# Kernel tuning notes

Measured on AMD Instinct MI355X. Metric: run time of the kernel, lower is better.

## Reference

```python
import jax, jax.numpy as jnp
import numpy as np

N_NODES = 100000
N_EDGES = 1600000
D = 64
N_LAYERS = 3
N_GRAPHS = 128
BN_EPS = 1e-5


def setup_inputs() -> dict:
    key = jax.random.key(0)
    k_x, k_e, k_b, k_w = jax.random.split(key, 4)
    x = jax.random.normal(k_x, (N_NODES, D), dtype=jnp.float32)
    edge_index = jax.random.randint(k_e, (2, N_EDGES), 0, N_NODES, dtype=jnp.int64)
    batch = jnp.sort(jax.random.randint(k_b, (N_NODES,), 0, N_GRAPHS, dtype=jnp.int64))
    Ws = jax.random.normal(k_w, (N_LAYERS, D, D), dtype=jnp.float32) * (1.0 / np.sqrt(D))
    bs = jnp.zeros((N_LAYERS, D), dtype=jnp.float32)
    gammas = jnp.ones((N_LAYERS, D), dtype=jnp.float32)
    betas = jnp.zeros((N_LAYERS, D), dtype=jnp.float32)
    return {"x": x, "edge_index": edge_index, "batch": batch,
            "Ws": Ws, "bs": bs, "gammas": gammas, "betas": betas}


def reference(x, edge_index, batch, Ws, bs, gammas, betas):
    N = x.shape[0]
    # GCN: add self-loops, symmetric normalization deg^{-1/2}_src * deg^{-1/2}_dst
    loop = jnp.arange(N, dtype=edge_index.dtype)
    src = jnp.concatenate([edge_index[0], loop])  # [E+N]
    dst = jnp.concatenate([edge_index[1], loop])
    deg = jax.ops.segment_sum(jnp.ones_like(dst, dtype=x.dtype), dst, num_segments=N)
    dinv = jnp.where(deg > 0, jax.lax.rsqrt(deg), 0.0)
    norm = dinv[src] * dinv[dst]  # [E+N]

    h = x
    for l in range(N_LAYERS):
        t = h @ Ws[l]                                    # [N,D] dense transform
        msg = t[src] * norm[:, None]                     # gather + scale [E+N,D]
        t = jax.ops.segment_sum(msg, dst, num_segments=N) + bs[l]
        # BatchNorm1d (training-style batch statistics, biased variance)
        mean = jnp.mean(t, axis=0)
        var = jnp.mean((t - mean) ** 2, axis=0)
        t = (t - mean) * jax.lax.rsqrt(var + BN_EPS) * gammas[l] + betas[l]
        h = jax.nn.relu(t)

    # global mean pool over graphs
    sums = jax.ops.segment_sum(h, batch, num_segments=N_GRAPHS)        # [G,D]
    counts = jax.ops.segment_sum(jnp.ones((N,), dtype=h.dtype), batch, num_segments=N_GRAPHS)
    return sums / jnp.maximum(counts, 1.0)[:, None]
```

## Files before the change

kernel.cpp:

```cpp
#include <hip/hip_runtime.h>
#include <hip/hip_bf16.h>

typedef __hip_bfloat16 bf16;
typedef short bf16x8 __attribute__((ext_vector_type(8)));
typedef float f32x4 __attribute__((ext_vector_type(4)));

#define NN 100000
#define NE 1600000
#define DD 64
#define NL 3
#define NG 128
#define BN_EPS 1e-5f
#define SCAN_BLK 98
#define TILE_ROWS 64
#define LSW 72
#define NT ((NN + TILE_ROWS - 1) / TILE_ROWS)
#define GB_NODES 48
#define GB_BLOCKS ((NN + GB_NODES - 1) / GB_NODES)
#define ECAP 1664
#define CSW_CAP (NE + 7 * NN)

__global__ __launch_bounds__(256) void detect_kernel(const int* __restrict__ ei,
                                                     const int* __restrict__ batch,
                                                     int* __restrict__ flags) {
    __shared__ int s_e, s_b;
    if (threadIdx.x == 0) { s_e = 0; s_b = 0; }
    __syncthreads();
    for (int i = threadIdx.x; i < 512; i += 256) {
        if (ei[2 * i + 1] != 0) atomicOr(&s_e, 1);
        if (batch[NN - 1024 + 2 * i + 1] != 0) atomicOr(&s_b, 1);
    }
    __syncthreads();
    if (threadIdx.x == 0) { flags[0] = s_e; flags[1] = s_b; }
}

__device__ __forceinline__ int ld_src(const int* ei, int e, int is32) {
    return is32 ? ei[e] : ei[2 * e];
}
__device__ __forceinline__ int ld_dst(const int* ei, int e, int is32) {
    return is32 ? ei[NE + e] : ei[2 * NE + 2 * e];
}
__device__ __forceinline__ int ld_batch(const int* b, int n, int is32) {
    return is32 ? b[n] : b[2 * n];
}
__device__ __forceinline__ float bf2f(unsigned short u) {
    return __uint_as_float(((unsigned int)u) << 16);
}
__device__ __forceinline__ unsigned short f2bf(float x) {
    bf16 b = __float2bfloat16(x);
    return *reinterpret_cast<unsigned short*>(&b);
}
__device__ __forceinline__ void split_bf16(float x, unsigned short& hi, unsigned short& lo) {
    hi = f2bf(x);
    lo = f2bf(x - bf2f(hi));
}
__device__ __forceinline__ int pad8(int d) { return (d + 7) & ~7; }

__global__ __launch_bounds__(256) void deg_kernel(const int* __restrict__ ei,
                                                  const int* __restrict__ flags,
                                                  int* __restrict__ deg_cnt) {
    int is32 = flags[0];
    int e = blockIdx.x * 256 + threadIdx.x;
    if (e < NE) atomicAdd(&deg_cnt[ld_dst(ei, e, is32)], 1);
}

__global__ __launch_bounds__(256) void scan_part_kernel(const int* __restrict__ deg_cnt,
                                                        int* __restrict__ blocksum,
                                                        float* __restrict__ dinv) {
    __shared__ int s[256];
    int base = blockIdx.x * 1024 + threadIdx.x * 4;
    int t = 0;
    if (base < NN) {
        int4 v = *(const int4*)(deg_cnt + base);
        t = pad8(v.x) + pad8(v.y) + pad8(v.z) + pad8(v.w);
        float4 dv = make_float4(rsqrtf((float)v.x + 1.f), rsqrtf((float)v.y + 1.f),
                                rsqrtf((float)v.z + 1.f), rsqrtf((float)v.w + 1.f));
        *(float4*)(dinv + base) = dv;
    }
    s[threadIdx.x] = t;
    __syncthreads();
    for (int off = 128; off > 0; off >>= 1) {
        if (threadIdx.x < off) s[threadIdx.x] += s[threadIdx.x + off];
        __syncthreads();
    }
    if (threadIdx.x == 0) blocksum[blockIdx.x] = s[0];
}

__global__ __launch_bounds__(256) void scan_write_kernel(int* __restrict__ deg_cnt,
                                                         const int* __restrict__ blocksum,
                                                         int* __restrict__ rowptr) {
    __shared__ int sb[128];
    __shared__ int s[256];
    if (threadIdx.x < 128)
        sb[threadIdx.x] = (threadIdx.x < SCAN_BLK) ? blocksum[threadIdx.x] : 0;
    __syncthreads();
    for (int off = 1; off < 128; off <<= 1) {
        int a = 0;
        if (threadIdx.x < 128 && threadIdx.x >= off) a = sb[threadIdx.x - off];
        __syncthreads();
        if (threadIdx.x < 128) sb[threadIdx.x] += a;
        __syncthreads();
    }
    int blockpre = (blockIdx.x == 0) ? 0 : sb[blockIdx.x - 1];
    if (blockIdx.x == SCAN_BLK - 1 && threadIdx.x == 0)
        rowptr[NN] = sb[SCAN_BLK - 1];

    int base = blockIdx.x * 1024 + threadIdx.x * 4;
    int4 v = make_int4(0, 0, 0, 0);
    if (base < NN) v = *(const int4*)(deg_cnt + base);
    int p0 = pad8(v.x), p1 = pad8(v.y), p2 = pad8(v.z), p3 = pad8(v.w);
    int t = p0 + p1 + p2 + p3;
    s[threadIdx.x] = t;
    for (int off = 1; off < 256; off <<= 1) {
        __syncthreads();
        int a = (threadIdx.x >= off) ? s[threadIdx.x - off] : 0;
        __syncthreads();
        s[threadIdx.x] += a;
    }
    __syncthreads();
    int pre = blockpre + s[threadIdx.x] - t;
    if (base < NN) {
        rowptr[base] = pre;
        rowptr[base + 1] = pre + p0;
        rowptr[base + 2] = pre + p0 + p1;
        rowptr[base + 3] = pre + p0 + p1 + p2;
        *(int4*)(deg_cnt + base) = make_int4(0, 0, 0, 0);
    }
}

__global__ __launch_bounds__(256) void fill_kernel(const int* __restrict__ ei,
                                                   const int* __restrict__ flags,
                                                   const float* __restrict__ dinv,
                                                   const int* __restrict__ rowptr,
                                                   int* __restrict__ cursor,
                                                   int2* __restrict__ csw) {
    int is32 = flags[0];
    int e = blockIdx.x * 256 + threadIdx.x;
    if (e >= NE) return;
    int s = ld_src(ei, e, is32), d = ld_dst(ei, e, is32);
    int pos = rowptr[d] + atomicAdd(&cursor[d], 1);
    float w = dinv[s] * dinv[d];
    csw[pos] = make_int2(s << 7, __float_as_int(w));
}

__global__ __launch_bounds__(256) void gemm_kernel(const float* __restrict__ h,
                                                   const float* __restrict__ W,
                                                   const float* __restrict__ accum_prev,
                                                   const float* __restrict__ gamma,
                                                   const float* __restrict__ beta,
                                                   int use_bn, float alpha,
                                                   bf16* __restrict__ t,
                                                   float* __restrict__ accum_l) {
    if (blockIdx.x == 0 && threadIdx.x < 128) accum_l[threadIdx.x] = 0.f;

    __shared__ unsigned short ls_hi[TILE_ROWS * LSW];
    __shared__ unsigned short ls_lo[TILE_ROWS * LSW];
    __shared__ float ssc[DD], ssh[DD];
    int tid = threadIdx.x;
    if (tid < 64) {
        if (use_bn) {
            float S = accum_prev[tid], Q = accum_prev[64 + tid];
            float mean = S / (float)NN;
            float var = fmaxf(Q / (float)NN - mean * mean, 0.f);
            float sc = gamma[tid] * rsqrtf(var + BN_EPS);
            ssc[tid] = sc;
            ssh[tid] = beta[tid] - mean * sc;
        } else {
            ssc[tid] = 1.f;
            ssh[tid] = 0.f;
        }
    }

    int lane = tid & 63;
    int wv = tid >> 6;
    int lr = lane & 15;
    int lg = lane >> 4;

    bf16x8 bhi[2][4], blo[2][4];
#pragma unroll
    for (int ks = 0; ks < 2; ++ks)
#pragma unroll
        for (int nt = 0; nt < 4; ++nt)
#pragma unroll
            for (int e = 0; e < 8; ++e) {
                float wval = W[(ks * 32 + lg * 8 + e) * DD + nt * 16 + lr];
                unsigned short hi, lo;
                split_bf16(wval, hi, lo);
                bhi[ks][nt][e] = (short)hi;
                blo[ks][nt][e] = (short)lo;
            }
    __syncthreads();

    for (int tile = blockIdx.x; tile < NT; tile += gridDim.x) {
        int row0 = tile * TILE_ROWS;
        int nrows = min(TILE_ROWS, NN - row0);
#pragma unroll
        for (int it = 0; it < 4; ++it) {
            int flat = (tid + it * 256) * 4;
            int gflat = row0 * DD + flat;
            if (gflat < NN * DD) {
                float4 hv = *(const float4*)(h + gflat);
                int c0 = flat & 63;
                float4 s4 = *(const float4*)(ssc + c0);
                float4 b4 = *(const float4*)(ssh + c0);
                float x0 = hv.x * s4.x + b4.x;
                float x1 = hv.y * s4.y + b4.y;
                float x2 = hv.z * s4.z + b4.z;
                float x3 = hv.w * s4.w + b4.w;
                x0 = fmaxf(x0, x0 * alpha);
                x1 = fmaxf(x1, x1 * alpha);
                x2 = fmaxf(x2, x2 * alpha);
                x3 = fmaxf(x3, x3 * alpha);
                unsigned short h0, l0, h1, l1, h2, l2, h3, l3;
                split_bf16(x0, h0, l0);
                split_bf16(x1, h1, l1);
                split_bf16(x2, h2, l2);
                split_bf16(x3, h3, l3);
                int row = flat >> 6;
                *(ushort4*)(ls_hi + row * LSW + c0) = make_ushort4(h0, h1, h2, h3);
                *(ushort4*)(ls_lo + row * LSW + c0) = make_ushort4(l0, l1, l2, l3);
            }
        }
        __syncthreads();

        f32x4 acc[4];
#pragma unroll
        for (int nt = 0; nt < 4; ++nt) acc[nt] = (f32x4){0.f, 0.f, 0.f, 0.f};

#pragma unroll
        for (int ks = 0; ks < 2; ++ks) {
            int aoff = (wv * 16 + lr) * LSW + ks * 32 + lg * 8;
            bf16x8 a_hi = *(const bf16x8*)(ls_hi + aoff);
            bf16x8 a_lo = *(const bf16x8*)(ls_lo + aoff);
#pragma unroll
            for (int nt = 0; nt < 4; ++nt) {
                acc[nt] = __builtin_amdgcn_mfma_f32_16x16x32_bf16(a_hi, bhi[ks][nt],
                                                                  acc[nt], 0, 0, 0);
                acc[nt] = __builtin_amdgcn_mfma_f32_16x16x32_bf16(a_hi, blo[ks][nt],
                                                                  acc[nt], 0, 0, 0);
                acc[nt] = __builtin_amdgcn_mfma_f32_16x16x32_bf16(a_lo, bhi[ks][nt],
                                                                  acc[nt], 0, 0, 0);
            }
        }
        __syncthreads();

#pragma unroll
        for (int nt = 0; nt < 4; ++nt)
#pragma unroll
            for (int rg = 0; rg < 4; ++rg) {
                int orow = wv * 16 + lg * 4 + rg;
                ls_hi[orow * LSW + nt * 16 + lr] = f2bf(acc[nt][rg]);
            }
        __syncthreads();
#pragma unroll
        for (int it = 0; it < 2; ++it) {
            int flat8 = (tid + it * 256) * 8;
            int row = flat8 >> 6, c = flat8 & 63;
            if (row < nrows) {
                uint4 v = *(const uint4*)(ls_hi + row * LSW + c);
                *(uint4*)((unsigned short*)t + (size_t)(row0 + row) * DD + c) = v;
            }
        }
        __syncthreads();
    }
}

__device__ __forceinline__ void batch8(const int2* __restrict__ ep, int j,
                                       const char* __restrict__ tbase, int f2,
                                       float& acc) {
    int2 a[8];
    unsigned short r[8];
#pragma unroll
    for (int u = 0; u < 8; ++u) a[u] = ep[j + u];
#pragma unroll
    for (int u = 0; u < 8; ++u)
        r[u] = *(const unsigned short*)(tbase + (unsigned)(a[u].x + f2));
#pragma unroll
    for (int u = 0; u < 8; ++u) acc += bf2f(r[u]) * __int_as_float(a[u].y);
}

__device__ __forceinline__ void batch8x2(const int2* __restrict__ ep, int jA, int jB,
                                         const char* __restrict__ tbase, int f2,
                                         float& accA, float& accB) {
    int2 aA[8], aB[8];
    unsigned short rA[8], rB[8];
#pragma unroll
    for (int u = 0; u < 8; ++u) { aA[u] = ep[jA + u]; aB[u] = ep[jB + u]; }
#pragma unroll
    for (int u = 0; u < 8; ++u) {
        rA[u] = *(const unsigned short*)(tbase + (unsigned)(aA[u].x + f2));
        rB[u] = *(const unsigned short*)(tbase + (unsigned)(aB[u].x + f2));
    }
#pragma unroll
    for (int u = 0; u < 8; ++u) {
        accA += bf2f(rA[u]) * __int_as_float(aA[u].y);
        accB += bf2f(rB[u]) * __int_as_float(aB[u].y);
    }
}

__device__ __forceinline__ void batch8x4(const int2* __restrict__ ep, int jA, int jB,
                                         int jC, int jD,
                                         const char* __restrict__ tbase, int f2,
                                         float& accA, float& accB, float& accC,
                                         float& accD) {
    int2 aA[8], aB[8], aC[8], aD[8];
    unsigned short rA[8], rB[8], rC[8], rD[8];
#pragma unroll
    for (int u = 0; u < 8; ++u) {
        aA[u] = ep[jA + u];
        aB[u] = ep[jB + u];
        aC[u] = ep[jC + u];
        aD[u] = ep[jD + u];
    }
#pragma unroll
    for (int u = 0; u < 8; ++u) {
        rA[u] = *(const unsigned short*)(tbase + (unsigned)(aA[u].x + f2));
        rB[u] = *(const unsigned short*)(tbase + (unsigned)(aB[u].x + f2));
        rC[u] = *(const unsigned short*)(tbase + (unsigned)(aC[u].x + f2));
        rD[u] = *(const unsigned short*)(tbase + (unsigned)(aD[u].x + f2));
    }
#pragma unroll
    for (int u = 0; u < 8; ++u) {
        accA += bf2f(rA[u]) * __int_as_float(aA[u].y);
        accB += bf2f(rB[u]) * __int_as_float(aB[u].y);
        accC += bf2f(rC[u]) * __int_as_float(aC[u].y);
        accD += bf2f(rD[u]) * __int_as_float(aD[u].y);
    }
}

__device__ __forceinline__ void run_quad(const int2* __restrict__ ep,
                                         const char* __restrict__ tbase, int f2,
                                         int jA, int eA, int jB, int eB,
                                         int jC, int eC, int jD, int eD,
                                         float& accA, float& accB, float& accC,
                                         float& accD) {
    while (jA < eA && jB < eB && jC < eC && jD < eD) {
        batch8x4(ep, jA, jB, jC, jD, tbase, f2, accA, accB, accC, accD);
        jA += 8; jB += 8; jC += 8; jD += 8;
    }
    while (jA < eA && jB < eB) { batch8x2(ep, jA, jB, tbase, f2, accA, accB); jA += 8; jB += 8; }
    while (jC < eC && jD < eD) { batch8x2(ep, jC, jD, tbase, f2, accC, accD); jC += 8; jD += 8; }
    while (jA < eA && jC < eC) { batch8x2(ep, jA, jC, tbase, f2, accA, accC); jA += 8; jC += 8; }
    while (jA < eA && jD < eD) { batch8x2(ep, jA, jD, tbase, f2, accA, accD); jA += 8; jD += 8; }
    while (jB < eB && jC < eC) { batch8x2(ep, jB, jC, tbase, f2, accB, accC); jB += 8; jC += 8; }
    while (jB < eB && jD < eD) { batch8x2(ep, jB, jD, tbase, f2, accB, accD); jB += 8; jD += 8; }
    while (jA < eA) { batch8(ep, jA, tbase, f2, accA); jA += 8; }
    while (jB < eB) { batch8(ep, jB, tbase, f2, accB); jB += 8; }
    while (jC < eC) { batch8(ep, jC, tbase, f2, accC); jC += 8; }
    while (jD < eD) { batch8(ep, jD, tbase, f2, accD); jD += 8; }
}

__global__ __launch_bounds__(256) void gather_kernel(const bf16* __restrict__ t,
                                                     const float* __restrict__ dinv,
                                                     const float* __restrict__ bias,
                                                     const int* __restrict__ rowptr,
                                                     const int2* __restrict__ csw,
                                                     float* __restrict__ h,
                                                     float* __restrict__ accum_l) {
    __shared__ int2 se[ECAP];
    __shared__ int srp[GB_NODES + 1];
    __shared__ float s_sum[256], s_sq[256];

    int f = threadIdx.x & 63;
    int wv = threadIdx.x >> 6;
    int nb0 = blockIdx.x * GB_NODES;
    int nloc = min(GB_NODES, NN - nb0);

    for (int i = threadIdx.x; i <= nloc; i += 256) srp[i] = rowptr[nb0 + i];
    __syncthreads();
    int ebase = srp[0];
    int nE = srp[nloc] - ebase;
    bool staged = (nE <= ECAP);
    int ncap = min(nE, ECAP);
    for (int i = threadIdx.x; i < ncap; i += 256) se[i] = csw[ebase + i];
    __syncthreads();

    const char* tbase = (const char*)t;
    int f2 = f * 2;
    const unsigned short* tf = (const unsigned short*)t + f;
    float bb = bias[f];
    float sum = 0.f, sq = 0.f;

    for (int q = wv; 4 * q < nloc; q += 4) {
        int d0 = 4 * q;
        int nA = nb0 + d0, nB = nA + 1, nC = nA + 2, nD = nA + 3;
        float diA = dinv[nA], diB = dinv[nB], diC = dinv[nC], diD = dinv[nD];
        float accA = bf2f(tf[(size_t)nA * DD]) * diA * diA + bb;
        float accB = bf2f(tf[(size_t)nB * DD]) * diB * diB + bb;
        float accC = bf2f(tf[(size_t)nC * DD]) * diC * diC + bb;
        float accD = bf2f(tf[(size_t)nD * DD]) * diD * diD + bb;
        int jA = srp[d0] - ebase, eA = srp[d0 + 1] - ebase;
        int jB = eA, eB = srp[d0 + 2] - ebase;
        int jC = eB, eC = srp[d0 + 3] - ebase;
        int jD = eC, eD = srp[d0 + 4] - ebase;

        if (staged)
            run_quad(se, tbase, f2, jA, eA, jB, eB, jC, eC, jD, eD, accA, accB, accC, accD);
        else
            run_quad(csw + ebase, tbase, f2, jA, eA, jB, eB, jC, eC, jD, eD,
                     accA, accB, accC, accD);

        h[(size_t)nA * DD + f] = accA;
        h[(size_t)nB * DD + f] = accB;
        h[(size_t)nC * DD + f] = accC;
        h[(size_t)nD * DD + f] = accD;
        sum += accA + accB + accC + accD;
        sq += accA * accA + accB * accB + accC * accC + accD * accD;
    }
    s_sum[threadIdx.x] = sum;
    s_sq[threadIdx.x] = sq;
    __syncthreads();
    if (threadIdx.x < 64) {
        sum = s_sum[f] + s_sum[64 + f] + s_sum[128 + f] + s_sum[192 + f];
        sq = s_sq[f] + s_sq[64 + f] + s_sq[128 + f] + s_sq[192 + f];
        atomicAdd(&accum_l[f], sum);
        atomicAdd(&accum_l[64 + f], sq);
    }
}

#define POOL_CHUNK 128
__global__ __launch_bounds__(256) void pool_kernel(const float* __restrict__ hraw,
                                                   const float* __restrict__ accum_l,
                                                   const float* __restrict__ gamma,
                                                   const float* __restrict__ beta,
                                                   const int* __restrict__ batch,
                                                   const int* __restrict__ flags,
                                                   float* __restrict__ pool,
                                                   float* __restrict__ counts) {
    __shared__ float ssc[64], ssh[64];
    if (threadIdx.x < 64) {
        float S = accum_l[threadIdx.x], Q = accum_l[64 + threadIdx.x];
        float mean = S / (float)NN;
        float var = fmaxf(Q / (float)NN - mean * mean, 0.f);
        float sc = gamma[threadIdx.x] * rsqrtf(var + BN_EPS);
        ssc[threadIdx.x] = sc;
        ssh[threadIdx.x] = beta[threadIdx.x] - mean * sc;
    }
    __syncthreads();
    int is32 = flags[1];
    int f = threadIdx.x & 63, rg = threadIdx.x >> 6;
    float sc = ssc[f], sh = ssh[f];
    int base = blockIdx.x * POOL_CHUNK;
    float acc = 0.f, cnt = 0.f;
    int cur = -1;
    for (int i = rg; i < POOL_CHUNK; i += 4) {
        int n = base + i;
        if (n >= NN) break;
        int g = ld_batch(batch, n, is32);
        if (g != cur) {
            if (cur >= 0) {
                atomicAdd(&pool[cur * DD + f], acc);
                if (f == 0) atomicAdd(&counts[cur], cnt);
            }
            acc = 0.f;
            cnt = 0.f;
            cur = g;
        }
        acc += fmaxf(hraw[(size_t)n * DD + f] * sc + sh, 0.f);
        cnt += 1.f;
    }
    if (cur >= 0) {
        atomicAdd(&pool[cur * DD + f], acc);
        if (f == 0) atomicAdd(&counts[cur], cnt);
    }
}

__global__ __launch_bounds__(256) void final_kernel(const float* __restrict__ pool,
                                                    const float* __restrict__ counts,
                                                    float* __restrict__ out) {
    int i = blockIdx.x * 256 + threadIdx.x;
    if (i < NG * DD) {
        int g = i >> 6;
        out[i] = pool[i] / fmaxf(counts[g], 1.0f);
    }
}

extern "C" void kernel_launch(void* const* d_in, const int* in_sizes, int n_in,
                              void* d_out, int out_size, void* d_ws, size_t ws_size,
                              hipStream_t stream) {
    const float* x = (const float*)d_in[0];
    const int* edge_index = (const int*)d_in[1];
    const int* batch = (const int*)d_in[2];
    const float* Ws = (const float*)d_in[3];
    const float* bs = (const float*)d_in[4];
    const float* gammas = (const float*)d_in[5];
    const float* betas = (const float*)d_in[6];
    float* out = (float*)d_out;

    float* h = (float*)d_ws;
    bf16* t = (bf16*)(h + (size_t)NN * DD);
    int2* csw = (int2*)(t + (size_t)NN * DD);
    float* dinv = (float*)(csw + CSW_CAP);
    int* deg_cnt = (int*)(dinv + NN);
    float* pool = (float*)(deg_cnt + NN);
    float* counts = pool + NG * DD;
    int* rowptr = (int*)(counts + NG);
    float* accum = (float*)(rowptr + NN + 1);
    int* flags = (int*)(accum + NL * 128);
    int* blocksum = flags + 2;

    hipMemsetAsync(deg_cnt, 0, (NN + NG * DD + NG) * sizeof(float), stream);
    hipMemsetAsync(csw, 0, (size_t)CSW_CAP * sizeof(int2), stream);

    detect_kernel<<<1, 256, 0, stream>>>(edge_index, batch, flags);
    deg_kernel<<<(NE + 255) / 256, 256, 0, stream>>>(edge_index, flags, deg_cnt);
    scan_part_kernel<<<SCAN_BLK, 256, 0, stream>>>(deg_cnt, blocksum, dinv);
    scan_write_kernel<<<SCAN_BLK, 256, 0, stream>>>(deg_cnt, blocksum, rowptr);
    fill_kernel<<<(NE + 255) / 256, 256, 0, stream>>>(edge_index, flags, dinv, rowptr,
                                                      deg_cnt, csw);

    for (int l = 0; l < NL; ++l) {
        const float* hin = (l == 0) ? x : h;
        float alpha = (l == 0) ? 1.0f : 0.0f;
        gemm_kernel<<<NT, 256, 0, stream>>>(hin, Ws + (size_t)l * DD * DD,
                                            accum + (l - 1 >= 0 ? l - 1 : 0) * 128,
                                            gammas + (l - 1 >= 0 ? l - 1 : 0) * DD,
                                            betas + (l - 1 >= 0 ? l - 1 : 0) * DD,
                                            (l > 0) ? 1 : 0, alpha, t, accum + l * 128);
        gather_kernel<<<GB_BLOCKS, 256, 0, stream>>>(t, dinv, bs + l * DD, rowptr, csw, h,
                                                     accum + l * 128);
    }

    pool_kernel<<<(NN + POOL_CHUNK - 1) / POOL_CHUNK, 256, 0, stream>>>(
        h, accum + 2 * 128, gammas + 2 * DD, betas + 2 * DD, batch, flags, pool, counts);
    final_kernel<<<(NG * DD + 255) / 256, 256, 0, stream>>>(pool, counts, out);
}
```

Baseline: 557.8 us.

## Factor GCN normalization into GEMM prescale and gather postscale, drop edge weights

Splits the symmetric normalization dinv[s]*dinv[d]: the GEMM epilogue scales each output row by dinv of the source, and the gather multiplies the summed neighbour row by dinv of the destination. This removes the per-edge weight, halving the CSR edge array to one int per edge and letting the gather load indices as int4 and do plain adds instead of FMAs with weights. Padding entries now point to a zeroed row placed before t, via the index offset s+1 and a tbase shifted back by 128 bytes. The cost is one extra per-row multiply in the GEMM and slightly different rounding, since the prescaled value is stored in bf16.

```diff
diff --git a/kernel.cpp b/kernel.cpp
--- a/kernel.cpp
+++ b/kernel.cpp
@@ -130,21 +130,20 @@
 
 __global__ __launch_bounds__(256) void fill_kernel(const int* __restrict__ ei,
                                                    const int* __restrict__ flags,
-                                                   const float* __restrict__ dinv,
                                                    const int* __restrict__ rowptr,
                                                    int* __restrict__ cursor,
-                                                   int2* __restrict__ csw) {
+                                                   int* __restrict__ csw) {
     int is32 = flags[0];
     int e = blockIdx.x * 256 + threadIdx.x;
     if (e >= NE) return;
     int s = ld_src(ei, e, is32), d = ld_dst(ei, e, is32);
     int pos = rowptr[d] + atomicAdd(&cursor[d], 1);
-    float w = dinv[s] * dinv[d];
-    csw[pos] = make_int2(s << 7, __float_as_int(w));
+    csw[pos] = (s + 1) << 7;
 }
 
 __global__ __launch_bounds__(256) void gemm_kernel(const float* __restrict__ h,
                                                    const float* __restrict__ W,
+                                                   const float* __restrict__ dinv,
                                                    const float* __restrict__ accum_prev,
                                                    const float* __restrict__ gamma,
                                                    const float* __restrict__ beta,
@@ -155,7 +154,7 @@
 
     __shared__ unsigned short ls_hi[TILE_ROWS * LSW];
     __shared__ unsigned short ls_lo[TILE_ROWS * LSW];
-    __shared__ float ssc[DD], ssh[DD];
+    __shared__ float ssc[DD], ssh[DD], sdinv[TILE_ROWS];
     int tid = threadIdx.x;
     if (tid < 64) {
         if (use_bn) {
@@ -194,6 +193,7 @@
     for (int tile = blockIdx.x; tile < NT; tile += gridDim.x) {
         int row0 = tile * TILE_ROWS;
         int nrows = min(TILE_ROWS, NN - row0);
+        if (tid < 64) sdinv[tid] = (row0 + tid < NN) ? dinv[row0 + tid] : 0.f;
 #pragma unroll
         for (int it = 0; it < 4; ++it) {
             int flat = (tid + it * 256) * 4;
@@ -249,7 +249,7 @@
 #pragma unroll
             for (int rg = 0; rg < 4; ++rg) {
                 int orow = wv * 16 + lg * 4 + rg;
-                ls_hi[orow * LSW + nt * 16 + lr] = f2bf(acc[nt][rg]);
+                ls_hi[orow * LSW + nt * 16 + lr] = f2bf(acc[nt][rg] * sdinv[orow]);
             }
         __syncthreads();
 #pragma unroll
@@ -265,70 +265,112 @@
     }
 }
 
-__device__ __forceinline__ void batch8(const int2* __restrict__ ep, int j,
+__device__ __forceinline__ void batch8(const int* __restrict__ ep, int j,
                                        const char* __restrict__ tbase, int f2,
                                        float& acc) {
-    int2 a[8];
+    int4 a0 = *(const int4*)(ep + j);
+    int4 a1 = *(const int4*)(ep + j + 4);
     unsigned short r[8];
-#pragma unroll
-    for (int u = 0; u < 8; ++u) a[u] = ep[j + u];
-#pragma unroll
-    for (int u = 0; u < 8; ++u)
-        r[u] = *(const unsigned short*)(tbase + (unsigned)(a[u].x + f2));
-#pragma unroll
-    for (int u = 0; u < 8; ++u) acc += bf2f(r[u]) * __int_as_float(a[u].y);
-}
-
-__device__ __forceinline__ void batch8x2(const int2* __restrict__ ep, int jA, int jB,
+    r[0] = *(const unsigned short*)(tbase + (unsigned)(a0.x + f2));
+    r[1] = *(const unsigned short*)(tbase + (unsigned)(a0.y + f2));
+    r[2] = *(const unsigned short*)(tbase + (unsigned)(a0.z + f2));
+    r[3] = *(const unsigned short*)(tbase + (unsigned)(a0.w + f2));
+    r[4] = *(const unsigned short*)(tbase + (unsigned)(a1.x + f2));
+    r[5] = *(const unsigned short*)(tbase + (unsigned)(a1.y + f2));
+    r[6] = *(const unsigned short*)(tbase + (unsigned)(a1.z + f2));
+    r[7] = *(const unsigned short*)(tbase + (unsigned)(a1.w + f2));
+    float s01 = bf2f(r[0]) + bf2f(r[1]), s23 = bf2f(r[2]) + bf2f(r[3]);
+    float s45 = bf2f(r[4]) + bf2f(r[5]), s67 = bf2f(r[6]) + bf2f(r[7]);
+    acc += (s01 + s23) + (s45 + s67);
+}
+
+__device__ __forceinline__ void batch8x2(const int* __restrict__ ep, int jA, int jB,
                                          const char* __restrict__ tbase, int f2,
                                          float& accA, float& accB) {
-    int2 aA[8], aB[8];
+    int4 aA0 = *(const int4*)(ep + jA), aA1 = *(const int4*)(ep + jA + 4);
+    int4 aB0 = *(const int4*)(ep + jB), aB1 = *(const int4*)(ep + jB + 4);
     unsigned short rA[8], rB[8];
-#pragma unroll
-    for (int u = 0; u < 8; ++u) { aA[u] = ep[jA + u]; aB[u] = ep[jB + u]; }
-#pragma unroll
-    for (int u = 0; u < 8; ++u) {
-        rA[u] = *(const unsigned short*)(tbase + (unsigned)(aA[u].x + f2));
-        rB[u] = *(const unsigned short*)(tbase + (unsigned)(aB[u].x + f2));
-    }
-#pragma unroll
-    for (int u = 0; u < 8; ++u) {
-        accA += bf2f(rA[u]) * __int_as_float(aA[u].y);
-        accB += bf2f(rB[u]) * __int_as_float(aB[u].y);
-    }
-}
-
-__device__ __forceinline__ void batch8x4(const int2* __restrict__ ep, int jA, int jB,
+    rA[0] = *(const unsigned short*)(tbase + (unsigned)(aA0.x + f2));
+    rA[1] = *(const unsigned short*)(tbase + (unsigned)(aA0.y + f2));
+    rA[2] = *(const unsigned short*)(tbase + (unsigned)(aA0.z + f2));
+    rA[3] = *(const unsigned short*)(tbase + (unsigned)(aA0.w + f2));
+    rA[4] = *(const unsigned short*)(tbase + (unsigned)(aA1.x + f2));
+    rA[5] = *(const unsigned short*)(tbase + (unsigned)(aA1.y + f2));
+    rA[6] = *(const unsigned short*)(tbase + (unsigned)(aA1.z + f2));
+    rA[7] = *(const unsigned short*)(tbase + (unsigned)(aA1.w + f2));
+    rB[0] = *(const unsigned short*)(tbase + (unsigned)(aB0.x + f2));
+    rB[1] = *(const unsigned short*)(tbase + (unsigned)(aB0.y + f2));
+    rB[2] = *(const unsigned short*)(tbase + (unsigned)(aB0.z + f2));
+    rB[3] = *(const unsigned short*)(tbase + (unsigned)(aB0.w + f2));
+    rB[4] = *(const unsigned short*)(tbase + (unsigned)(aB1.x + f2));
+    rB[5] = *(const unsigned short*)(tbase + (unsigned)(aB1.y + f2));
+    rB[6] = *(const unsigned short*)(tbase + (unsigned)(aB1.z + f2));
+    rB[7] = *(const unsigned short*)(tbase + (unsigned)(aB1.w + f2));
+    float sA01 = bf2f(rA[0]) + bf2f(rA[1]), sA23 = bf2f(rA[2]) + bf2f(rA[3]);
+    float sA45 = bf2f(rA[4]) + bf2f(rA[5]), sA67 = bf2f(rA[6]) + bf2f(rA[7]);
+    accA += (sA01 + sA23) + (sA45 + sA67);
+    float sB01 = bf2f(rB[0]) + bf2f(rB[1]), sB23 = bf2f(rB[2]) + bf2f(rB[3]);
+    float sB45 = bf2f(rB[4]) + bf2f(rB[5]), sB67 = bf2f(rB[6]) + bf2f(rB[7]);
+    accB += (sB01 + sB23) + (sB45 + sB67);
+}
+
+__device__ __forceinline__ void batch8x4(const int* __restrict__ ep, int jA, int jB,
                                          int jC, int jD,
                                          const char* __restrict__ tbase, int f2,
                                          float& accA, float& accB, float& accC,
                                          float& accD) {
-    int2 aA[8], aB[8], aC[8], aD[8];
+    int4 aA0 = *(const int4*)(ep + jA), aA1 = *(const int4*)(ep + jA + 4);
+    int4 aB0 = *(const int4*)(ep + jB), aB1 = *(const int4*)(ep + jB + 4);
+    int4 aC0 = *(const int4*)(ep + jC), aC1 = *(const int4*)(ep + jC + 4);
+    int4 aD0 = *(const int4*)(ep + jD), aD1 = *(const int4*)(ep + jD + 4);
     unsigned short rA[8], rB[8], rC[8], rD[8];
-#pragma unroll
-    for (int u = 0; u < 8; ++u) {
-        aA[u] = ep[jA + u];
-        aB[u] = ep[jB + u];
-        aC[u] = ep[jC + u];
-        aD[u] = ep[jD + u];
-    }
-#pragma unroll
-    for (int u = 0; u < 8; ++u) {
-        rA[u] = *(const unsigned short*)(tbase + (unsigned)(aA[u].x + f2));
-        rB[u] = *(const unsigned short*)(tbase + (unsigned)(aB[u].x + f2));
-        rC[u] = *(const unsigned short*)(tbase + (unsigned)(aC[u].x + f2));
-        rD[u] = *(const unsigned short*)(tbase + (unsigned)(aD[u].x + f2));
-    }
-#pragma unroll
-    for (int u = 0; u < 8; ++u) {
-        accA += bf2f(rA[u]) * __int_as_float(aA[u].y);
-        accB += bf2f(rB[u]) * __int_as_float(aB[u].y);
-        accC += bf2f(rC[u]) * __int_as_float(aC[u].y);
-        accD += bf2f(rD[u]) * __int_as_float(aD[u].y);
-    }
-}
-
-__device__ __forceinline__ void run_quad(const int2* __restrict__ ep,
+    rA[0] = *(const unsigned short*)(tbase + (unsigned)(aA0.x + f2));
+    rA[1] = *(const unsigned short*)(tbase + (unsigned)(aA0.y + f2));
+    rA[2] = *(const unsigned short*)(tbase + (unsigned)(aA0.z + f2));
+    rA[3] = *(const unsigned short*)(tbase + (unsigned)(aA0.w + f2));
+    rA[4] = *(const unsigned short*)(tbase + (unsigned)(aA1.x + f2));
+    rA[5] = *(const unsigned short*)(tbase + (unsigned)(aA1.y + f2));
+    rA[6] = *(const unsigned short*)(tbase + (unsigned)(aA1.z + f2));
+    rA[7] = *(const unsigned short*)(tbase + (unsigned)(aA1.w + f2));
+    rB[0] = *(const unsigned short*)(tbase + (unsigned)(aB0.x + f2));
+    rB[1] = *(const unsigned short*)(tbase + (unsigned)(aB0.y + f2));
+    rB[2] = *(const unsigned short*)(tbase + (unsigned)(aB0.z + f2));
+    rB[3] = *(const unsigned short*)(tbase + (unsigned)(aB0.w + f2));
+    rB[4] = *(const unsigned short*)(tbase + (unsigned)(aB1.x + f2));
+    rB[5] = *(const unsigned short*)(tbase + (unsigned)(aB1.y + f2));
+    rB[6] = *(const unsigned short*)(tbase + (unsigned)(aB1.z + f2));
+    rB[7] = *(const unsigned short*)(tbase + (unsigned)(aB1.w + f2));
+    rC[0] = *(const unsigned short*)(tbase + (unsigned)(aC0.x + f2));
+    rC[1] = *(const unsigned short*)(tbase + (unsigned)(aC0.y + f2));
+    rC[2] = *(const unsigned short*)(tbase + (unsigned)(aC0.z + f2));
+    rC[3] = *(const unsigned short*)(tbase + (unsigned)(aC0.w + f2));
+    rC[4] = *(const unsigned short*)(tbase + (unsigned)(aC1.x + f2));
+    rC[5] = *(const unsigned short*)(tbase + (unsigned)(aC1.y + f2));
+    rC[6] = *(const unsigned short*)(tbase + (unsigned)(aC1.z + f2));
+    rC[7] = *(const unsigned short*)(tbase + (unsigned)(aC1.w + f2));
+    rD[0] = *(const unsigned short*)(tbase + (unsigned)(aD0.x + f2));
+    rD[1] = *(const unsigned short*)(tbase + (unsigned)(aD0.y + f2));
+    rD[2] = *(const unsigned short*)(tbase + (unsigned)(aD0.z + f2));
+    rD[3] = *(const unsigned short*)(tbase + (unsigned)(aD0.w + f2));
+    rD[4] = *(const unsigned short*)(tbase + (unsigned)(aD1.x + f2));
+    rD[5] = *(const unsigned short*)(tbase + (unsigned)(aD1.y + f2));
+    rD[6] = *(const unsigned short*)(tbase + (unsigned)(aD1.z + f2));
+    rD[7] = *(const unsigned short*)(tbase + (unsigned)(aD1.w + f2));
+    float sA01 = bf2f(rA[0]) + bf2f(rA[1]), sA23 = bf2f(rA[2]) + bf2f(rA[3]);
+    float sA45 = bf2f(rA[4]) + bf2f(rA[5]), sA67 = bf2f(rA[6]) + bf2f(rA[7]);
+    accA += (sA01 + sA23) + (sA45 + sA67);
+    float sB01 = bf2f(rB[0]) + bf2f(rB[1]), sB23 = bf2f(rB[2]) + bf2f(rB[3]);
+    float sB45 = bf2f(rB[4]) + bf2f(rB[5]), sB67 = bf2f(rB[6]) + bf2f(rB[7]);
+    accB += (sB01 + sB23) + (sB45 + sB67);
+    float sC01 = bf2f(rC[0]) + bf2f(rC[1]), sC23 = bf2f(rC[2]) + bf2f(rC[3]);
+    float sC45 = bf2f(rC[4]) + bf2f(rC[5]), sC67 = bf2f(rC[6]) + bf2f(rC[7]);
+    accC += (sC01 + sC23) + (sC45 + sC67);
+    float sD01 = bf2f(rD[0]) + bf2f(rD[1]), sD23 = bf2f(rD[2]) + bf2f(rD[3]);
+    float sD45 = bf2f(rD[4]) + bf2f(rD[5]), sD67 = bf2f(rD[6]) + bf2f(rD[7]);
+    accD += (sD01 + sD23) + (sD45 + sD67);
+}
+
+__device__ __forceinline__ void run_quad(const int* __restrict__ ep,
                                          const char* __restrict__ tbase, int f2,
                                          int jA, int eA, int jB, int eB,
                                          int jC, int eC, int jD, int eD,
@@ -354,10 +396,10 @@
                                                      const float* __restrict__ dinv,
                                                      const float* __restrict__ bias,
                                                      const int* __restrict__ rowptr,
-                                                     const int2* __restrict__ csw,
+                                                     const int* __restrict__ csw,
                                                      float* __restrict__ h,
                                                      float* __restrict__ accum_l) {
-    __shared__ int2 se[ECAP];
+    __shared__ __attribute__((aligned(16))) int se[ECAP];
     __shared__ int srp[GB_NODES + 1];
     __shared__ float s_sum[256], s_sq[256];
 
@@ -371,11 +413,13 @@
     int ebase = srp[0];
     int nE = srp[nloc] - ebase;
     bool staged = (nE <= ECAP);
-    int ncap = min(nE, ECAP);
-    for (int i = threadIdx.x; i < ncap; i += 256) se[i] = csw[ebase + i];
-    __syncthreads();
-
-    const char* tbase = (const char*)t;
+    if (staged) {
+        for (int i = threadIdx.x * 4; i < nE; i += 1024)
+            *(int4*)(se + i) = *(const int4*)(csw + ebase + i);
+    }
+    __syncthreads();
+
+    const char* tbase = (const char*)t - 128;
     int f2 = f * 2;
     const unsigned short* tf = (const unsigned short*)t + f;
     float bb = bias[f];
@@ -384,11 +428,10 @@
     for (int q = wv; 4 * q < nloc; q += 4) {
         int d0 = 4 * q;
         int nA = nb0 + d0, nB = nA + 1, nC = nA + 2, nD = nA + 3;
-        float diA = dinv[nA], diB = dinv[nB], diC = dinv[nC], diD = dinv[nD];
-        float accA = bf2f(tf[(size_t)nA * DD]) * diA * diA + bb;
-        float accB = bf2f(tf[(size_t)nB * DD]) * diB * diB + bb;
-        float accC = bf2f(tf[(size_t)nC * DD]) * diC * diC + bb;
-        float accD = bf2f(tf[(size_t)nD * DD]) * diD * diD + bb;
+        float accA = bf2f(tf[(size_t)nA * DD]);
+        float accB = bf2f(tf[(size_t)nB * DD]);
+        float accC = bf2f(tf[(size_t)nC * DD]);
+        float accD = bf2f(tf[(size_t)nD * DD]);
         int jA = srp[d0] - ebase, eA = srp[d0 + 1] - ebase;
         int jB = eA, eB = srp[d0 + 2] - ebase;
         int jC = eB, eC = srp[d0 + 3] - ebase;
@@ -400,6 +443,11 @@
             run_quad(csw + ebase, tbase, f2, jA, eA, jB, eB, jC, eC, jD, eD,
                      accA, accB, accC, accD);
 
+        float diA = dinv[nA], diB = dinv[nB], diC = dinv[nC], diD = dinv[nD];
+        accA = accA * diA + bb;
+        accB = accB * diB + bb;
+        accC = accC * diC + bb;
+        accD = accD * diD + bb;
         h[(size_t)nA * DD + f] = accA;
         h[(size_t)nB * DD + f] = accB;
         h[(size_t)nC * DD + f] = accC;
@@ -488,8 +536,9 @@
     float* out = (float*)d_out;
 
     float* h = (float*)d_ws;
-    bf16* t = (bf16*)(h + (size_t)NN * DD);
-    int2* csw = (int2*)(t + (size_t)NN * DD);
+    bf16* zrow = (bf16*)(h + (size_t)NN * DD);
+    bf16* t = zrow + DD;
+    int* csw = (int*)(t + (size_t)NN * DD);
     float* dinv = (float*)(csw + CSW_CAP);
     int* deg_cnt = (int*)(dinv + NN);
     float* pool = (float*)(deg_cnt + NN);
@@ -500,19 +549,20 @@
     int* blocksum = flags + 2;
 
     hipMemsetAsync(deg_cnt, 0, (NN + NG * DD + NG) * sizeof(float), stream);
-    hipMemsetAsync(csw, 0, (size_t)CSW_CAP * sizeof(int2), stream);
+    hipMemsetAsync(csw, 0, (size_t)CSW_CAP * sizeof(int), stream);
+    hipMemsetAsync(zrow, 0, DD * sizeof(bf16), stream);
 
     detect_kernel<<<1, 256, 0, stream>>>(edge_index, batch, flags);
     deg_kernel<<<(NE + 255) / 256, 256, 0, stream>>>(edge_index, flags, deg_cnt);
     scan_part_kernel<<<SCAN_BLK, 256, 0, stream>>>(deg_cnt, blocksum, dinv);
     scan_write_kernel<<<SCAN_BLK, 256, 0, stream>>>(deg_cnt, blocksum, rowptr);
-    fill_kernel<<<(NE + 255) / 256, 256, 0, stream>>>(edge_index, flags, dinv, rowptr,
+    fill_kernel<<<(NE + 255) / 256, 256, 0, stream>>>(edge_index, flags, rowptr,
                                                       deg_cnt, csw);
 
     for (int l = 0; l < NL; ++l) {
         const float* hin = (l == 0) ? x : h;
         float alpha = (l == 0) ? 1.0f : 0.0f;
-        gemm_kernel<<<NT, 256, 0, stream>>>(hin, Ws + (size_t)l * DD * DD,
+        gemm_kernel<<<NT, 256, 0, stream>>>(hin, Ws + (size_t)l * DD * DD, dinv,
                                             accum + (l - 1 >= 0 ? l - 1 : 0) * 128,
                                             gammas + (l - 1 >= 0 ? l - 1 : 0) * DD,
                                             betas + (l - 1 >= 0 ? l - 1 : 0) * DD,
```

After: 594.5 us. +6.6%, slower.
